# Kernel tuning notes

Hardware: AMD Instinct MI355X
Metric: run time of the kernel (lower is better)

## Reference

```python
import jax, jax.numpy as jnp
import numpy as np

B, S, E, H = 4, 1024, 1024, 16
D = E // H          # head_dim = 64
ROT = 32            # rotary dims (first ROT channels of each head)


def _rope(x, freqs):
    # x: [B, H, S, D]; freqs: [1, 1, S, ROT]
    r = freqs.shape[-1]
    xl, xr = x[..., :r], x[..., r:]
    half = r // 2
    rot = jnp.concatenate([-xl[..., half:], xl[..., :half]], axis=-1)  # rotate_half
    xl = xl * jnp.cos(freqs) + rot * jnp.sin(freqs)
    return jnp.concatenate([xl, xr], axis=-1)


def setup_inputs() -> dict:
    key = jax.random.key(0)
    ks = jax.random.split(key, 7)
    std = 0.02
    return {
        "hidden_states": jax.random.normal(ks[0], (B, S, E), jnp.float32),
        "rotary_pos_emb": jax.random.normal(ks[1], (1, S, ROT), jnp.float32),
        "q_w": jax.random.normal(ks[2], (E, E), jnp.float32) * std,
        "k_w": jax.random.normal(ks[3], (E, E), jnp.float32) * std,
        "v_w": jax.random.normal(ks[4], (E, E), jnp.float32) * std,
        "o_w": jax.random.normal(ks[5], (E, E), jnp.float32) * std,
        "o_b": jnp.zeros((E,), jnp.float32),
    }


def reference(hidden_states, rotary_pos_emb, q_w, k_w, v_w, o_w, o_b):
    bsz, tgt_len, embed_dim = hidden_states.shape
    scale = D ** -0.5

    def shape(t):  # [B, S, E] -> [B, H, S, D]
        return t.reshape(bsz, tgt_len, H, D).transpose(0, 2, 1, 3)

    q = shape(hidden_states @ q_w.T * scale)
    k = shape(hidden_states @ k_w.T)
    v = shape(hidden_states @ v_w.T)

    freqs = rotary_pos_emb[:, None, :, :]  # [1, 1, S, ROT]
    q = _rope(q, freqs)
    k = _rope(k, freqs)
    v = _rope(v, freqs)

    attn = jnp.einsum("bhqd,bhkd->bhqk", q, k)
    causal = jnp.tril(jnp.ones((tgt_len, tgt_len), bool))
    attn = jnp.where(causal, attn, jnp.finfo(attn.dtype).min)
    attn = jax.nn.softmax(attn, axis=-1)

    out = jnp.einsum("bhqk,bhkd->bhqd", attn, v)
    out = out.transpose(0, 2, 1, 3).reshape(bsz, tgt_len, embed_dim)
    return out @ o_w.T + o_b
```

## Files before the change

kernel.cpp:

```cpp
#include <hip/hip_runtime.h>
#include <hip/hip_bf16.h>

typedef __bf16 bf16;
typedef __attribute__((ext_vector_type(2))) __bf16 bf16x2;
typedef __attribute__((ext_vector_type(4))) __bf16 bf16x4;
typedef __attribute__((ext_vector_type(8))) __bf16 bf16x8;
typedef __attribute__((ext_vector_type(4))) float f32x4;

#define NB 4
#define NS 1024
#define NE 1024
#define NH 16
#define ND 64
#define NROT 32
#define NM (NB*NS)

__device__ __forceinline__ void gload_lds16(const bf16* g, void* l) {
  __builtin_amdgcn_global_load_lds(
      (const __attribute__((address_space(1))) unsigned int*)g,
      (__attribute__((address_space(3))) unsigned int*)l,
      16, 0, 0);
}

struct PrepArgs {
  const float* w0; const float* w1; const float* w2; const float* w3;
  bf16* b0; bf16* b1; bf16* b2; bf16* b3;
  const float* hs; bf16* hb;
  const float* rot; float* ct; float* st;
};
__global__ void k_prep(PrepArgs a) {
  const int y = blockIdx.y;
  const int i = blockIdx.x * 256 + threadIdx.x;
  if (y < 4) {
    const float* s = (y == 0) ? a.w0 : (y == 1) ? a.w1 : (y == 2) ? a.w2 : a.w3;
    bf16* d = (y == 0) ? a.b0 : (y == 1) ? a.b1 : (y == 2) ? a.b2 : a.b3;
    float4 v = reinterpret_cast<const float4*>(s)[i];
    bf16x4 o = { (bf16)v.x, (bf16)v.y, (bf16)v.z, (bf16)v.w };
    *reinterpret_cast<bf16x4*>(d + (size_t)i * 4) = o;
  } else if (y < 8) {
    size_t off = (size_t)(y - 4) * (NM * NE / 16);
    float4 v = reinterpret_cast<const float4*>(a.hs)[off + i];
    bf16x4 o = { (bf16)v.x, (bf16)v.y, (bf16)v.z, (bf16)v.w };
    *reinterpret_cast<bf16x4*>(a.hb + (off + i) * 4) = o;
  } else {
    if (i < NS * NROT) {
      float v = a.rot[i];
      a.ct[i] = cosf(v);
      a.st[i] = sinf(v);
    }
  }
}

template<bool SWAP>
__device__ __forceinline__ void gemm_core256(
    const bf16* __restrict__ A, const bf16* __restrict__ W,
    bf16* lA, bf16* lB, int m0, int n0, f32x4 (&acc)[32])
{
  const int tid = threadIdx.x;
  const int wave = tid >> 6, lane = tid & 63;
  const int wm = wave >> 2, wn = wave & 3;
  const int fr = lane & 15, kg = lane >> 4;
  const int lrow8 = lane >> 3, lslot = lane & 7;

  auto stageH = [&](int kt, int c, int h) {
    const bf16* src = (h < 2) ? A : W;
    bf16* dst = (h < 2) ? lA : lB;
    const int base0 = (h < 2) ? m0 : n0;
    const int hh = h & 1;
#pragma unroll
    for (int i = 0; i < 2; ++i) {
      int chunk = hh * 16 + i * 8 + wave;
      int row = (chunk << 3) + lrow8;
      int slot = lslot ^ (row & 7);
      gload_lds16(src + (size_t)(base0 + row) * NE + kt + slot * 8,
                  (char*)dst + c * 32768 + chunk * 1024);
    }
  };

#pragma unroll
  for (int h = 0; h < 4; ++h) stageH(0, 0, h);
  asm volatile("s_waitcnt vmcnt(0)\n\ts_barrier" ::: "memory");

  constexpr int NT = NE / 64;
  bf16x8 bfrag[4][2];

  for (int t = 0; t < NT; ++t) {
    const int c = t & 1;
    const char* cA = (const char*)lA + c * 32768;
    const char* cB = (const char*)lB + c * 32768;

#pragma unroll
    for (int q = 0; q < 4; ++q) {
      if (t + 1 < NT) stageH((t + 1) * 64, c ^ 1, q);

      if (q == 0) {
        if (t > 0) {
          if (t + 1 < NT)
            asm volatile("s_waitcnt vmcnt(2)\n\ts_barrier" ::: "memory");
          else
            asm volatile("s_waitcnt vmcnt(0)\n\ts_barrier" ::: "memory");
        }
#pragma unroll
        for (int j = 0; j < 4; ++j) {
          int rb = wn * 64 + j * 16 + fr;
#pragma unroll
          for (int kk = 0; kk < 2; ++kk)
            bfrag[j][kk] = *reinterpret_cast<const bf16x8*>(
                cB + rb * 128 + (((kg + 4 * kk) ^ (rb & 7)) << 4));
        }
      }

      bf16x8 af[2][2];
#pragma unroll
      for (int u = 0; u < 2; ++u) {
        int ra = wm * 128 + (2 * q + u) * 16 + fr;
#pragma unroll
        for (int kk = 0; kk < 2; ++kk)
          af[u][kk] = *reinterpret_cast<const bf16x8*>(
              cA + ra * 128 + (((kg + 4 * kk) ^ (ra & 7)) << 4));
      }

      __builtin_amdgcn_sched_barrier(0);
      __builtin_amdgcn_s_setprio(1);
#pragma unroll
      for (int kk = 0; kk < 2; ++kk)
#pragma unroll
        for (int u = 0; u < 2; ++u)
#pragma unroll
          for (int j = 0; j < 4; ++j) {
            const int i = 2 * q + u;
            if constexpr (SWAP)
              acc[j * 8 + i] = __builtin_amdgcn_mfma_f32_16x16x32_bf16(
                  bfrag[j][kk], af[u][kk], acc[j * 8 + i], 0, 0, 0);
            else
              acc[i * 4 + j] = __builtin_amdgcn_mfma_f32_16x16x32_bf16(
                  af[u][kk], bfrag[j][kk], acc[i * 4 + j], 0, 0, 0);
          }
      __builtin_amdgcn_s_setprio(0);
      __builtin_amdgcn_sched_barrier(0);
    }

    asm volatile("s_waitcnt lgkmcnt(0)\n\ts_barrier" ::: "memory");
  }
}

__global__ __launch_bounds__(512) void k_proj(
    const bf16* __restrict__ A, const bf16* __restrict__ Wq, const bf16* __restrict__ Wk,
    const bf16* __restrict__ Wv, bf16* __restrict__ Oq, bf16* __restrict__ Ok,
    bf16* __restrict__ vt, const float* __restrict__ ct, const float* __restrict__ st)
{
  __shared__ bf16 lA[2 * 256 * 64];
  __shared__ bf16 lB[2 * 256 * 64];
  const int z = blockIdx.z;
  const int m0 = blockIdx.x * 256, n0 = blockIdx.y * 256;
  const int tid = threadIdx.x;
  const int wave = tid >> 6, lane = tid & 63;
  const int wm = wave >> 2, wn = wave & 3;
  const int fr = lane & 15, kg = lane >> 4;

  f32x4 acc[32] = {};

  if (z == 2) {
    gemm_core256<true>(A, Wv, lA, lB, m0, n0, acc);

    const int b = m0 >> 10;
    const int h = (n0 + wn * 64) >> 6;
    bf16* vtb = vt + ((size_t)(b * 16 + h)) * ND * NS;
#pragma unroll
    for (int i = 0; i < 8; ++i) {
      int sl = (m0 & (NS - 1)) + wm * 128 + i * 16 + fr;
#pragma unroll
      for (int r = 0; r < 4; ++r) {
        int dbase = kg * 4 + r;
        float x0 = acc[0 * 8 + i][r];
        float x1 = acc[1 * 8 + i][r];
        float c0 = ct[sl * NROT + dbase],      sn0 = st[sl * NROT + dbase];
        float c1 = ct[sl * NROT + 16 + dbase], sn1 = st[sl * NROT + 16 + dbase];
        float y0 = x0 * c0 - x1 * sn0;
        float y1 = x1 * c1 + x0 * sn1;
        vtb[(size_t)(dbase)      * NS + sl] = (bf16)y0;
        vtb[(size_t)(16 + dbase) * NS + sl] = (bf16)y1;
        vtb[(size_t)(32 + dbase) * NS + sl] = (bf16)acc[2 * 8 + i][r];
        vtb[(size_t)(48 + dbase) * NS + sl] = (bf16)acc[3 * 8 + i][r];
      }
    }
  } else {
    const bf16* W = (z == 0) ? Wq : Wk;
    bf16* Og = (z == 0) ? Oq : Ok;
    const float scale = (z == 0) ? 0.125f * 1.44269504f : 1.0f;

    gemm_core256<false>(A, W, lA, lB, m0, n0, acc);

#pragma unroll
    for (int i = 0; i < 8; ++i) {
      int rowbase = m0 + wm * 128 + i * 16 + kg * 4;
#pragma unroll
      for (int r = 0; r < 4; ++r) {
        int gm = rowbase + r;
        int s = gm & (NS - 1);
        float x0 = acc[i * 4 + 0][r] * scale;
        float x1 = acc[i * 4 + 1][r] * scale;
        float c0 = ct[s * NROT + fr],      sn0 = st[s * NROT + fr];
        float c1 = ct[s * NROT + 16 + fr], sn1 = st[s * NROT + 16 + fr];
        float y0 = x0 * c0 - x1 * sn0;
        float y1 = x1 * c1 + x0 * sn1;
        size_t rb = (size_t)gm * NE + n0 + wn * 64;
        Og[rb + 0 * 16 + fr] = (bf16)y0;
        Og[rb + 1 * 16 + fr] = (bf16)y1;
        Og[rb + 2 * 16 + fr] = (bf16)(acc[i * 4 + 2][r] * scale);
        Og[rb + 3 * 16 + fr] = (bf16)(acc[i * 4 + 3][r] * scale);
      }
    }
  }
}

template<int BM, int BN>
__device__ __forceinline__ void gemm_core(
    const bf16* __restrict__ A, const bf16* __restrict__ W,
    bf16* lA, bf16* lB, int m0, int n0, f32x4 (&acc)[BM/32][BN/32])
{
  const int tid = threadIdx.x;
  const int wave = tid >> 6, lane = tid & 63;
  const int wm = wave >> 1, wn = wave & 1;
  const int fr = lane & 15, kg = lane >> 4;

  const int sline = lane >> 3;
  const int lsl   = (lane & 7) ^ sline;
  const int srow  = 2 * sline + (lsl >> 2);
  const int skcol = (lsl & 3) * 8;
  constexpr int ACH = BM / 64;
  constexpr int BCH = BN / 64;
  constexpr int NSTAGE = ACH + BCH;

  auto stage = [&](int kt, int c) {
#pragma unroll
    for (int i = 0; i < ACH; ++i) {
      int chunk = i * 4 + wave;
      gload_lds16(A + (size_t)(m0 + chunk * 16 + srow) * NE + kt + skcol,
                  (char*)lA + c * (BM * 64) + chunk * 1024);
    }
#pragma unroll
    for (int i = 0; i < BCH; ++i) {
      int chunk = i * 4 + wave;
      gload_lds16(W + (size_t)(n0 + chunk * 16 + srow) * NE + kt + skcol,
                  (char*)lB + c * (BN * 64) + chunk * 1024);
    }
  };

  auto foff = [&](int ra) {
    return (ra >> 1) * 128 + (((((ra & 1) << 2) + kg) ^ ((ra >> 1) & 7)) << 4);
  };

  stage(0, 0);

  for (int kt = 0; kt < NE / 32; ++kt) {
    const int c = kt & 1;
    if (kt + 1 < NE / 32) {
      stage((kt + 1) * 32, c ^ 1);
      asm volatile("s_waitcnt vmcnt(%0)\n\ts_barrier" :: "n"(NSTAGE) : "memory");
    } else {
      asm volatile("s_waitcnt vmcnt(0)\n\ts_barrier" ::: "memory");
    }

    const char* cA = (const char*)lA + c * (BM * 64);
    const char* cB = (const char*)lB + c * (BN * 64);
    bf16x8 af[BM / 32], bfr[BN / 32];
#pragma unroll
    for (int i = 0; i < BM / 32; ++i)
      af[i] = *reinterpret_cast<const bf16x8*>(cA + foff(wm * (BM / 2) + i * 16 + fr));
#pragma unroll
    for (int j = 0; j < BN / 32; ++j)
      bfr[j] = *reinterpret_cast<const bf16x8*>(cB + foff(wn * (BN / 2) + j * 16 + fr));
#pragma unroll
    for (int i = 0; i < BM / 32; ++i)
#pragma unroll
      for (int j = 0; j < BN / 32; ++j)
        acc[i][j] = __builtin_amdgcn_mfma_f32_16x16x32_bf16(af[i], bfr[j], acc[i][j], 0, 0, 0);
    asm volatile("s_waitcnt lgkmcnt(0)\n\ts_barrier" ::: "memory");
  }
}

__global__ __launch_bounds__(256) void k_gemm_o(
    const bf16* __restrict__ A, const bf16* __restrict__ W, float* __restrict__ Og,
    const float* __restrict__ bias)
{
  __shared__ bf16 lA[2 * 64 * 32];
  __shared__ bf16 lB[2 * 128 * 32];
  const int m0 = blockIdx.x * 64, n0 = blockIdx.y * 128;
  f32x4 acc[2][4] = {};
  gemm_core<64, 128>(A, W, lA, lB, m0, n0, acc);

  const int tid = threadIdx.x;
  const int wave = tid >> 6, lane = tid & 63;
  const int wm = wave >> 1, wn = wave & 1;
  const int fr = lane & 15, kg = lane >> 4;
#pragma unroll
  for (int i = 0; i < 2; ++i)
#pragma unroll
    for (int j = 0; j < 4; ++j) {
      int gc = n0 + wn * 64 + j * 16 + fr;
      float bv = bias[gc];
#pragma unroll
      for (int r = 0; r < 4; ++r) {
        int gm = m0 + wm * 32 + i * 16 + kg * 4 + r;
        Og[(size_t)gm * NE + gc] = acc[i][j][r] + bv;
      }
    }
}

__global__ __launch_bounds__(256) void k_attn(
    const bf16* __restrict__ Q, const bf16* __restrict__ K,
    const bf16* __restrict__ VT, bf16* __restrict__ O)
{
  __shared__ bf16 lK[2][64 * 64];
  __shared__ bf16 lVT[64 * 64];
  __shared__ bf16 lP[4][16 * 68];
  const int tid = threadIdx.x;
  const int wave = tid >> 6, lane = tid & 63;
  const int fr = lane & 15, kg = lane >> 4;

  const int qt = 15 - (blockIdx.y >> 3);
  const int bh = blockIdx.x | ((blockIdx.y & 7) << 3);
  const int b = bh >> 4, h = bh & 15;
  const int nt = qt + 1;
  const bf16* Qb  = Q + (size_t)b * NS * NE + h * 64;
  const bf16* Kb  = K + (size_t)b * NS * NE + h * 64;
  const bf16* VTb = VT + (size_t)bh * ND * NS;
  bf16* Ob = O + (size_t)b * NS * NE + h * 64;

  const int qrow0 = qt * 64 + wave * 16;

  bf16x8 qf[2];
#pragma unroll
  for (int kk = 0; kk < 2; ++kk)
    qf[kk] = *reinterpret_cast<const bf16x8*>(
        Qb + (size_t)(qrow0 + fr) * NE + kk * 32 + kg * 8);

  const int srow = lane >> 3;
  const int sslot = (lane & 7) ^ srow;
  const int r0 = wave * 8 + srow;
  const int r1 = (wave + 4) * 8 + srow;
  const bf16* kA0 = Kb + (size_t)r0 * NE + sslot * 8;
  const bf16* kA1 = Kb + (size_t)r1 * NE + sslot * 8;
  const bf16* vA0 = VTb + (size_t)r0 * NS + sslot * 8;
  const bf16* vA1 = VTb + (size_t)r1 * NS + sslot * 8;
  char* ldsKa[2] = { (char*)lK[0] + wave * 1024, (char*)lK[1] + wave * 1024 };
  char* ldsKb[2] = { (char*)lK[0] + (wave + 4) * 1024, (char*)lK[1] + (wave + 4) * 1024 };
  char* ldsVa  = (char*)lVT + wave * 1024;
  char* ldsVb  = (char*)lVT + (wave + 4) * 1024;

  float m_ = -3.0e38f, l_ = 0.f;
  f32x4 oacc[4] = {};

  gload_lds16(kA0, ldsKa[0]);
  gload_lds16(kA1, ldsKb[0]);
  __syncthreads();

  for (int t = 0; t < nt; ++t) {
    const int c = t & 1;
    gload_lds16(vA0 + t * 64, ldsVa);
    gload_lds16(vA1 + t * 64, ldsVb);
    if (t + 1 < nt) {
      gload_lds16(kA0 + (size_t)(t + 1) * 64 * NE, ldsKa[c ^ 1]);
      gload_lds16(kA1 + (size_t)(t + 1) * 64 * NE, ldsKb[c ^ 1]);
    }

    const bf16* lKc = lK[c];
    f32x4 sacc[4] = {};
    __builtin_amdgcn_s_setprio(1);
#pragma unroll
    for (int kk = 0; kk < 2; ++kk)
#pragma unroll
      for (int j = 0; j < 4; ++j) {
        int rc = j * 16 + fr;
        bf16x8 kf = *reinterpret_cast<const bf16x8*>(
            lKc + rc * 64 + (((kg + 4 * kk) ^ (rc & 7)) << 3));
        sacc[j] = __builtin_amdgcn_mfma_f32_16x16x32_bf16(kf, qf[kk], sacc[j], 0, 0, 0);
      }
    __builtin_amdgcn_s_setprio(0);

    if (t == qt) {
      const int ql = wave * 16 + fr;
#pragma unroll
      for (int j = 0; j < 4; ++j)
#pragma unroll
        for (int r = 0; r < 4; ++r)
          if (16 * j + 4 * kg + r > ql) sacc[j][r] = -3.0e38f;
    }

    float m4 = fmaxf(fmaxf(fmaxf(sacc[0][0], sacc[0][1]), fmaxf(sacc[0][2], sacc[0][3])),
                     fmaxf(fmaxf(sacc[1][0], sacc[1][1]), fmaxf(sacc[1][2], sacc[1][3])));
    m4 = fmaxf(m4, fmaxf(fmaxf(fmaxf(sacc[2][0], sacc[2][1]), fmaxf(sacc[2][2], sacc[2][3])),
                         fmaxf(fmaxf(sacc[3][0], sacc[3][1]), fmaxf(sacc[3][2], sacc[3][3]))));
    m4 = fmaxf(m4, __shfl_xor(m4, 16));
    m4 = fmaxf(m4, __shfl_xor(m4, 32));

    if (!__all(m4 - m_ <= 8.0f)) {
      float nm = fmaxf(m_, m4);
      float corr = exp2f(m_ - nm);
      m_ = nm;
      l_ *= corr;
#pragma unroll
      for (int r = 0; r < 4; ++r) {
        float cr = __shfl(corr, kg * 4 + r);
#pragma unroll
        for (int df = 0; df < 4; ++df) oacc[df][r] *= cr;
      }
    }

    float ps = 0.f;
#pragma unroll
    for (int j = 0; j < 4; ++j) {
      float p0 = exp2f(sacc[j][0] - m_);
      float p1 = exp2f(sacc[j][1] - m_);
      float p2 = exp2f(sacc[j][2] - m_);
      float p3 = exp2f(sacc[j][3] - m_);
      ps += (p0 + p1) + (p2 + p3);
      bf16x4 pp = { (bf16)p0, (bf16)p1, (bf16)p2, (bf16)p3 };
      *reinterpret_cast<bf16x4*>(&lP[wave][fr * 68 + j * 16 + kg * 4]) = pp;
    }
    ps += __shfl_xor(ps, 16);
    ps += __shfl_xor(ps, 32);
    l_ += ps;

    __syncthreads();

    __builtin_amdgcn_s_setprio(1);
#pragma unroll
    for (int ks = 0; ks < 2; ++ks) {
      bf16x8 pf = *reinterpret_cast<const bf16x8*>(&lP[wave][fr * 68 + ks * 32 + kg * 8]);
#pragma unroll
      for (int df = 0; df < 4; ++df) {
        int d = df * 16 + fr;
        bf16x8 vf = *reinterpret_cast<const bf16x8*>(
            (const bf16*)lVT + d * 64 + (((kg + 4 * ks) ^ (d & 7)) << 3));
        oacc[df] = __builtin_amdgcn_mfma_f32_16x16x32_bf16(pf, vf, oacc[df], 0, 0, 0);
      }
    }
    __builtin_amdgcn_s_setprio(0);

    __syncthreads();
  }

  float linv[4];
#pragma unroll
  for (int r = 0; r < 4; ++r) linv[r] = 1.0f / __shfl(l_, kg * 4 + r);
#pragma unroll
  for (int df = 0; df < 4; ++df)
#pragma unroll
    for (int r = 0; r < 4; ++r)
      Ob[(size_t)(qrow0 + kg * 4 + r) * NE + df * 16 + fr] = (bf16)(oacc[df][r] * linv[r]);
}

extern "C" void kernel_launch(void* const* d_in, const int* in_sizes, int n_in,
                              void* d_out, int out_size, void* d_ws, size_t ws_size,
                              hipStream_t stream) {
  const float* hs  = (const float*)d_in[0];
  const float* rot = (const float*)d_in[1];
  const float* qw  = (const float*)d_in[2];
  const float* kw  = (const float*)d_in[3];
  const float* vw  = (const float*)d_in[4];
  const float* ow  = (const float*)d_in[5];
  const float* obb = (const float*)d_in[6];
  float* out = (float*)d_out;

  char* ws = (char*)d_ws;
  size_t off = 0;
  bf16* hb  = (bf16*)(ws + off); off += (size_t)NM * NE * 2;
  bf16* wqb = (bf16*)(ws + off); off += (size_t)NE * NE * 2;
  bf16* wkb = (bf16*)(ws + off); off += (size_t)NE * NE * 2;
  bf16* wvb = (bf16*)(ws + off); off += (size_t)NE * NE * 2;
  bf16* wob = (bf16*)(ws + off); off += (size_t)NE * NE * 2;
  bf16* qb  = (bf16*)(ws + off); off += (size_t)NM * NE * 2;
  bf16* kb  = (bf16*)(ws + off); off += (size_t)NM * NE * 2;
  bf16* vt  = (bf16*)(ws + off); off += (size_t)NM * NE * 2;
  float* ct = (float*)(ws + off); off += (size_t)NS * NROT * 4;
  float* st = (float*)(ws + off); off += (size_t)NS * NROT * 4;
  bf16* aob = hb;

  PrepArgs pa = { qw, kw, vw, ow, wqb, wkb, wvb, wob, hs, hb, rot, ct, st };
  k_prep<<<dim3(NE * NE / 4 / 256, 9), dim3(256), 0, stream>>>(pa);

  k_proj<<<dim3(NM / 256, NE / 256, 3), dim3(512), 0, stream>>>(
      hb, wqb, wkb, wvb, qb, kb, vt, ct, st);

  k_attn<<<dim3(8, 128), dim3(256), 0, stream>>>(qb, kb, vt, aob);

  k_gemm_o<<<dim3(NM / 64, NE / 128), dim3(256), 0, stream>>>(aob, wob, out, obb);

  (void)in_sizes; (void)n_in; (void)out_size; (void)ws_size;
}
```

Measured before the change: 101.7 us.

## Use single-buffered 64-wide K tiles in output projection GEMM

New measurement: 96.61 us. -5.0%, faster.

```diff
diff --git a/kernel.cpp b/kernel.cpp
--- a/kernel.cpp
+++ b/kernel.cpp
@@ -214,86 +214,59 @@
   }
 }
 
-template<int BM, int BN>
-__device__ __forceinline__ void gemm_core(
-    const bf16* __restrict__ A, const bf16* __restrict__ W,
-    bf16* lA, bf16* lB, int m0, int n0, f32x4 (&acc)[BM/32][BN/32])
+__global__ __launch_bounds__(256) void k_gemm_o(
+    const bf16* __restrict__ A, const bf16* __restrict__ W, float* __restrict__ Og,
+    const float* __restrict__ bias)
 {
+  __shared__ bf16 lA[64 * 64];
+  __shared__ bf16 lB[128 * 64];
+  const int m0 = blockIdx.x * 64, n0 = blockIdx.y * 128;
   const int tid = threadIdx.x;
   const int wave = tid >> 6, lane = tid & 63;
   const int wm = wave >> 1, wn = wave & 1;
   const int fr = lane & 15, kg = lane >> 4;
-
-  const int sline = lane >> 3;
-  const int lsl   = (lane & 7) ^ sline;
-  const int srow  = 2 * sline + (lsl >> 2);
-  const int skcol = (lsl & 3) * 8;
-  constexpr int ACH = BM / 64;
-  constexpr int BCH = BN / 64;
-  constexpr int NSTAGE = ACH + BCH;
-
-  auto stage = [&](int kt, int c) {
-#pragma unroll
-    for (int i = 0; i < ACH; ++i) {
+  const int lrow8 = lane >> 3, lslot = lane & 7;
+
+  f32x4 acc[2][4] = {};
+
+  for (int kt = 0; kt < NE; kt += 64) {
+#pragma unroll
+    for (int i = 0; i < 2; ++i) {
       int chunk = i * 4 + wave;
-      gload_lds16(A + (size_t)(m0 + chunk * 16 + srow) * NE + kt + skcol,
-                  (char*)lA + c * (BM * 64) + chunk * 1024);
-    }
-#pragma unroll
-    for (int i = 0; i < BCH; ++i) {
+      int row = (chunk << 3) + lrow8;
+      int slot = lslot ^ (row & 7);
+      gload_lds16(A + (size_t)(m0 + row) * NE + kt + slot * 8, (char*)lA + chunk * 1024);
+    }
+#pragma unroll
+    for (int i = 0; i < 4; ++i) {
       int chunk = i * 4 + wave;
-      gload_lds16(W + (size_t)(n0 + chunk * 16 + srow) * NE + kt + skcol,
-                  (char*)lB + c * (BN * 64) + chunk * 1024);
-    }
-  };
-
-  auto foff = [&](int ra) {
-    return (ra >> 1) * 128 + (((((ra & 1) << 2) + kg) ^ ((ra >> 1) & 7)) << 4);
-  };
-
-  stage(0, 0);
-
-  for (int kt = 0; kt < NE / 32; ++kt) {
-    const int c = kt & 1;
-    if (kt + 1 < NE / 32) {
-      stage((kt + 1) * 32, c ^ 1);
-      asm volatile("s_waitcnt vmcnt(%0)\n\ts_barrier" :: "n"(NSTAGE) : "memory");
-    } else {
-      asm volatile("s_waitcnt vmcnt(0)\n\ts_barrier" ::: "memory");
-    }
-
-    const char* cA = (const char*)lA + c * (BM * 64);
-    const char* cB = (const char*)lB + c * (BN * 64);
-    bf16x8 af[BM / 32], bfr[BN / 32];
-#pragma unroll
-    for (int i = 0; i < BM / 32; ++i)
-      af[i] = *reinterpret_cast<const bf16x8*>(cA + foff(wm * (BM / 2) + i * 16 + fr));
-#pragma unroll
-    for (int j = 0; j < BN / 32; ++j)
-      bfr[j] = *reinterpret_cast<const bf16x8*>(cB + foff(wn * (BN / 2) + j * 16 + fr));
-#pragma unroll
-    for (int i = 0; i < BM / 32; ++i)
-#pragma unroll
-      for (int j = 0; j < BN / 32; ++j)
-        acc[i][j] = __builtin_amdgcn_mfma_f32_16x16x32_bf16(af[i], bfr[j], acc[i][j], 0, 0, 0);
-    asm volatile("s_waitcnt lgkmcnt(0)\n\ts_barrier" ::: "memory");
+      int row = (chunk << 3) + lrow8;
+      int slot = lslot ^ (row & 7);
+      gload_lds16(W + (size_t)(n0 + row) * NE + kt + slot * 8, (char*)lB + chunk * 1024);
+    }
+    __syncthreads();
+#pragma unroll
+    for (int kk = 0; kk < 2; ++kk) {
+      bf16x8 af[2], bfr[4];
+#pragma unroll
+      for (int i = 0; i < 2; ++i) {
+        int ra = wm * 32 + i * 16 + fr;
+        af[i] = *reinterpret_cast<const bf16x8*>(lA + ra * 64 + (((kg + 4 * kk) ^ (ra & 7)) << 3));
+      }
+#pragma unroll
+      for (int j = 0; j < 4; ++j) {
+        int rb = wn * 64 + j * 16 + fr;
+        bfr[j] = *reinterpret_cast<const bf16x8*>(lB + rb * 64 + (((kg + 4 * kk) ^ (rb & 7)) << 3));
+      }
+#pragma unroll
+      for (int i = 0; i < 2; ++i)
+#pragma unroll
+        for (int j = 0; j < 4; ++j)
+          acc[i][j] = __builtin_amdgcn_mfma_f32_16x16x32_bf16(af[i], bfr[j], acc[i][j], 0, 0, 0);
+    }
+    __syncthreads();
   }
-}
-
-__global__ __launch_bounds__(256) void k_gemm_o(
-    const bf16* __restrict__ A, const bf16* __restrict__ W, float* __restrict__ Og,
-    const float* __restrict__ bias)
-{
-  __shared__ bf16 lA[2 * 64 * 32];
-  __shared__ bf16 lB[2 * 128 * 32];
-  const int m0 = blockIdx.x * 64, n0 = blockIdx.y * 128;
-  f32x4 acc[2][4] = {};
-  gemm_core<64, 128>(A, W, lA, lB, m0, n0, acc);
-
-  const int tid = threadIdx.x;
-  const int wave = tid >> 6, lane = tid & 63;
-  const int wm = wave >> 1, wn = wave & 1;
-  const int fr = lane & 15, kg = lane >> 4;
+
 #pragma unroll
   for (int i = 0; i < 2; ++i)
 #pragma unroll
```
